# Performance work log

Measured on AMD Instinct MI355X. Metric: run time of the kernel, lower is better.

## Reference

```python
import jax, jax.numpy as jnp
import numpy as np
from jax import lax

# Faithful JAX translation of ConvAttention (enc=True, mask=False), the core
# kernel-headroom op of Conv_Transformer. Key observation: the per-(s,t)-pair
# conv2 over concat(Q[...,s], K[...,t]) is linear, so it decomposes exactly as
# conv(Q_s, W_q) + conv(K_t, W_k) + bias, where W_q/W_k are the first/second
# half of conv2's input channels. This reproduces the same math without
# materializing the [b, 2c, h, w, s, t] tensor or looping over time.

B, C, H, W, S = 4, 64, 64, 64, 20
K_SIZE = 3


def _conv_same(x, w):
    # x: [N, Cin, H, W], w: [Cout, Cin, kh, kw]
    return lax.conv_general_dilated(
        x, w, window_strides=(1, 1), padding='SAME',
        dimension_numbers=('NCHW', 'OIHW', 'NCHW'))


def setup_inputs() -> dict:
    key = jax.random.key(0)
    k1, k2, k3, k4, k5 = jax.random.split(key, 5)
    x = jax.random.normal(k1, (B, C, H, W, S), dtype=jnp.float32)
    w1 = jax.random.normal(k2, (3 * C, C, 1, 1), dtype=jnp.float32) * 0.05
    b1 = jax.random.normal(k3, (3 * C,), dtype=jnp.float32) * 0.05
    w2 = jax.random.normal(k4, (1, 2 * C, K_SIZE, K_SIZE), dtype=jnp.float32) * 0.05
    b2 = jax.random.normal(k5, (1,), dtype=jnp.float32) * 0.05
    return {'x': x, 'w1': w1, 'b1': b1, 'w2': w2, 'b2': b2}


def reference(x, w1, b1, w2, b2):
    b, c, h, w, s = x.shape
    # conv1 (1x1) per timestep -> QKV: [b, 3c, h, w, s]
    qkv = jnp.einsum('bchws,oc->bohws', x, w1[:, :, 0, 0]) \
        + b1[None, :, None, None, None]
    Q, K, V = jnp.split(qkv, 3, axis=1)  # each [b, c, h, w, s]

    # Decompose conv2 over concatenated channels.
    Wq, Wk = w2[:, :c], w2[:, c:]  # each [1, c, kh, kw]

    def per_time_conv(t5, wgt):
        # t5: [b, c, h, w, s] -> scores [b, h, w, s]
        flat = jnp.moveaxis(t5, -1, 1).reshape(b * s, c, h, w)
        out = _conv_same(flat, wgt)  # [b*s, 1, h, w]
        return out.reshape(b, s, h, w).transpose(0, 2, 3, 1)

    A = per_time_conv(Q, Wq)  # [b, h, w, s]  (query index)
    Bk = per_time_conv(K, Wk)  # [b, h, w, t]  (key index)

    # score[b,h,w,t,s] = conv2(concat(Q_s, K_t)) ; softmax over t (keys)
    scores = A[:, :, :, None, :] + Bk[:, :, :, :, None] + b2[0]
    attn = jax.nn.softmax(scores, axis=-2)  # [b, h, w, t, s]

    # V_out[b,c,h,w,s] = sum_t attn[...,t,s] * V[...,t]
    V_out = jnp.einsum('bhwts,bchwt->bchws', attn, V)
    return V_out
```

## Files before the change

kernel.cpp:

```cpp
#include <hip/hip_runtime.h>
#include <math.h>

#define Bb 4
#define Cc 64
#define Hh 64
#define Ww 64
#define Ss 20

constexpr int XC = Hh * Ww * Ss;
constexpr int XH = Ww * Ss;
constexpr int XW = Ss;
constexpr int XB = Cc * XC;
constexpr int NSITE = Bb * Hh * Ww;
constexpr int BKPLANE = NSITE * Ss;


__global__ void ct_fold_weights(const float* __restrict__ w1,
                                const float* __restrict__ b1,
                                const float* __restrict__ w2,
                                float* __restrict__ ws) {
    int tid = threadIdx.x;
    if (tid < 576) {
        int tap = tid >> 6, cp = tid & 63;
        float acc = 0.f;
        #pragma unroll 8
        for (int c = 0; c < 64; ++c)
            acc += w2[(64 + c) * 9 + tap] * w1[(64 + c) * 64 + cp];
        ws[tid] = acc;
    } else if (tid < 585) {
        int tap = tid - 576;
        float acc = 0.f;
        for (int c = 0; c < 64; ++c)
            acc += w2[(64 + c) * 9 + tap] * b1[64 + c];
        ws[576 + tap] = acc;
    }
}

template<int NPART>
__global__ __launch_bounds__(320) void ct_conv_bk(
        const float* __restrict__ x,
        const float* __restrict__ ws,
        float* __restrict__ bk) {
    __shared__ float weff[576];
    __shared__ float btap[9];
    int tid = threadIdx.x;
    for (int i = tid; i < 576; i += 320) weff[i] = ws[i];
    if (tid < 9) btap[tid] = ws[576 + tid];
    __syncthreads();

    constexpr int NCP = 64 / NPART;
    constexpr int CHUNK = 256 * NPART / 8;
    int g = (blockIdx.x & 7) * CHUNK + (blockIdx.x >> 3);
    int part = g >> 8;
    int nl = g & 255;
    int b = nl >> 6, h = nl & 63;
    int w = tid / 5, t4 = tid % 5;

    float vmask[9];
    int off[9];
    #pragma unroll
    for (int dh = 0; dh < 3; ++dh) {
        int hh = h + dh - 1;
        float hv = (hh >= 0 && hh < Hh) ? 1.f : 0.f;
        int hc = hh < 0 ? 0 : (hh > Hh - 1 ? Hh - 1 : hh);
        #pragma unroll
        for (int dw = 0; dw < 3; ++dw) {
            int wc = w + dw - 1;
            float wvd = (wc >= 0 && wc < Ww) ? 1.f : 0.f;
            int wcl = wc < 0 ? 0 : (wc > Ww - 1 ? Ww - 1 : wc);
            vmask[dh * 3 + dw] = hv * wvd;
            off[dh * 3 + dw] = hc * XH + wcl * XW;
        }
    }

    float bsum = 0.f;
    if (part == 0) {
        #pragma unroll
        for (int tap = 0; tap < 9; ++tap) bsum += btap[tap] * vmask[tap];
    }
    float4 acc = make_float4(bsum, bsum, bsum, bsum);

    const float* xb = x + b * XB + part * NCP * XC + t4 * 4;
    #pragma unroll 2
    for (int c = 0; c < NCP; ++c) {
        const float* xc = xb + c * XC;
        #pragma unroll
        for (int tap = 0; tap < 9; ++tap) {
            float wv = weff[tap * 64 + part * NCP + c] * vmask[tap];
            const float4 xv = *reinterpret_cast<const float4*>(xc + off[tap]);
            acc.x = fmaf(wv, xv.x, acc.x);
            acc.y = fmaf(wv, xv.y, acc.y);
            acc.z = fmaf(wv, xv.z, acc.z);
            acc.w = fmaf(wv, xv.w, acc.w);
        }
    }
    int site = nl * 64 + w;
    *reinterpret_cast<float4*>(bk + part * BKPLANE + site * 20 + t4 * 4) = acc;
}

template<int NPART>
__global__ __launch_bounds__(256) void ct_attn_out(
        const float* __restrict__ x,
        const float* __restrict__ w1,
        const float* __restrict__ b1,
        const float* __restrict__ bk,
        float* __restrict__ out) {
    __shared__ float w1t[64 * 65];
    __shared__ float psm[8][20];
    __shared__ float xsh[8][65];
    int tid = threadIdx.x;
    #pragma unroll
    for (int k = 0; k < 16; ++k) {
        int j = tid + k * 256;
        int r = j >> 6, q = j & 63;
        w1t[q * 65 + r] = w1[8192 + j];
    }

    int site0 = blockIdx.x * 8;

    if (tid < 160) {
        int si = tid / 20, i = tid % 20;
        float v = 0.f;
        #pragma unroll
        for (int pt = 0; pt < NPART; ++pt)
            v += bk[pt * BKPLANE + (site0 + si) * 20 + i];
        psm[si][i] = v;
    }
    __syncthreads();

    if (tid < 8) {
        float p[20];
        #pragma unroll
        for (int i = 0; i < 20; ++i) p[i] = psm[tid][i];
        float m = p[0];
        #pragma unroll
        for (int i = 1; i < 20; ++i) m = fmaxf(m, p[i]);
        float ssum = 0.f;
        #pragma unroll
        for (int i = 0; i < 20; ++i) { p[i] = __expf(p[i] - m); ssum += p[i]; }
        float inv = 1.f / ssum;
        #pragma unroll
        for (int i = 0; i < 20; ++i) psm[tid][i] = p[i] * inv;
    }
    __syncthreads();

    int si = tid & 7, cg = tid >> 3;
    int site = site0 + si;
    int b = site >> 12, hw = site & 4095;

    #pragma unroll
    for (int k = 0; k < 2; ++k) {
        int c = cg * 2 + k;
        const float* xp = x + (b * 64 + c) * XC + hw * 20;
        float xbv = 0.f;
        #pragma unroll
        for (int i = 0; i < 5; ++i) {
            float4 xv = reinterpret_cast<const float4*>(xp)[i];
            xbv = fmaf(psm[si][4 * i],     xv.x, xbv);
            xbv = fmaf(psm[si][4 * i + 1], xv.y, xbv);
            xbv = fmaf(psm[si][4 * i + 2], xv.z, xbv);
            xbv = fmaf(psm[si][4 * i + 3], xv.w, xbv);
        }
        xsh[si][c] = xbv;
    }
    __syncthreads();

    #pragma unroll
    for (int k = 0; k < 2; ++k) {
        int c = cg * 2 + k;
        float R = b1[128 + c];
        #pragma unroll 8
        for (int cp = 0; cp < 64; ++cp)
            R = fmaf(w1t[cp * 65 + c], xsh[si][cp], R);
        float* op = out + (b * 64 + c) * XC + hw * 20;
        float4 rv = make_float4(R, R, R, R);
        #pragma unroll
        for (int s4 = 0; s4 < 5; ++s4)
            reinterpret_cast<float4*>(op)[s4] = rv;
    }
}

extern "C" void kernel_launch(void* const* d_in, const int* in_sizes, int n_in,
                              void* d_out, int out_size, void* d_ws, size_t ws_size,
                              hipStream_t stream) {
    const float* x  = (const float*)d_in[0];
    const float* w1 = (const float*)d_in[1];
    const float* b1 = (const float*)d_in[2];
    const float* w2 = (const float*)d_in[3];
    float* ws    = (float*)d_ws;
    float* bkbuf = ws + 640;
    float* out   = (float*)d_out;

    ct_fold_weights<<<1, 640, 0, stream>>>(w1, b1, w2, ws);

    size_t need8 = (size_t)(640 + 8 * BKPLANE) * sizeof(float);
    size_t need4 = (size_t)(640 + 4 * BKPLANE) * sizeof(float);
    if (ws_size >= need8) {
        ct_conv_bk<8><<<2048, 320, 0, stream>>>(x, ws, bkbuf);
        ct_attn_out<8><<<2048, 256, 0, stream>>>(x, w1, b1, bkbuf, out);
    } else if (ws_size >= need4) {
        ct_conv_bk<4><<<1024, 320, 0, stream>>>(x, ws, bkbuf);
        ct_attn_out<4><<<2048, 256, 0, stream>>>(x, w1, b1, bkbuf, out);
    } else {
        ct_conv_bk<1><<<256, 320, 0, stream>>>(x, ws, bkbuf);
        ct_attn_out<1><<<2048, 256, 0, stream>>>(x, w1, b1, bkbuf, out);
    }
}
```

Before: 81.00 us.

## Replace 9-tap gather conv with row-streaming scatter conv over channel partitions

Adds a conv kernel that gives each block a 4-row strip of h. Every x row is loaded once and scattered into up to three output-row accumulators held in a register ring, instead of each output gathering nine taps with repeated loads. When the workspace is large enough it also splits channels into 16 partitions (4 channels each), so the partial sums are reduced in the attention kernel. This cuts redundant x loads in the conv but adds halo rows per strip and twice as many partial planes for the attention kernel to read.

New measurement: 73.81 us. 1.1x faster.

```diff
diff --git a/kernel.cpp b/kernel.cpp
--- a/kernel.cpp
+++ b/kernel.cpp
@@ -36,6 +36,106 @@
     }
 }
 
+template<int NCP>
+__global__ __launch_bounds__(320) void ct_conv_scatter(
+        const float* __restrict__ x,
+        const float* __restrict__ ws,
+        float* __restrict__ bk) {
+    constexpr int NPART = 64 / NCP;
+    constexpr int HT = 4;
+    constexpr int TOTAL = 4 * NPART * 16;
+    __shared__ float wsl[9 * NCP];
+    __shared__ float bt[9];
+    int tid = threadIdx.x;
+
+    int g = (blockIdx.x & 7) * (TOTAL / 8) + (blockIdx.x >> 3);
+    int hc = g & 15; g >>= 4;
+    int b = g & 3;
+    int part = g >> 2;
+
+    if (tid < 9 * NCP)
+        wsl[tid] = ws[(tid / NCP) * 64 + part * NCP + (tid % NCP)];
+    if (tid < 9) bt[tid] = ws[576 + tid];
+    __syncthreads();
+
+    int w = tid / 5, t4 = tid % 5;
+    int h0 = hc * HT;
+    float m0 = (w == 0)  ? 0.f : 1.f;
+    float m2 = (w == 63) ? 0.f : 1.f;
+    int wm1 = (w == 0) ? 0 : w - 1;
+    int wp1 = (w == 63) ? 63 : w + 1;
+    int cw0 = wm1 * XW, cw1 = w * XW, cw2 = wp1 * XW;
+
+    float bw0 = bt[0] * m0 + bt[1] + bt[2] * m2;
+    float bw1 = bt[3] * m0 + bt[4] + bt[5] * m2;
+    float bw2 = bt[6] * m0 + bt[7] + bt[8] * m2;
+    bool bias_on = (part == 0);
+
+    const float* xbase = x + b * XB + part * NCP * XC + t4 * 4;
+    float* bkp = bk + part * BKPLANE;
+
+    float4 ring[3];
+
+    #pragma unroll
+    for (int k = 0; k < HT + 2; ++k) {
+        if (k < HT) {
+            float bs = 0.f;
+            if (bias_on) {
+                int o = h0 + k;
+                bs = (o >= 1 ? bw0 : 0.f) + bw1 + (o + 1 < 64 ? bw2 : 0.f);
+            }
+            ring[k % 3] = make_float4(bs, bs, bs, bs);
+        }
+
+        int hr = h0 - 1 + k;
+        float4 xv[NCP][3];
+        if (hr >= 0 && hr < 64) {
+            #pragma unroll
+            for (int c = 0; c < NCP; ++c) {
+                const float* xr = xbase + c * XC + hr * XH;
+                xv[c][0] = *reinterpret_cast<const float4*>(xr + cw0);
+                xv[c][1] = *reinterpret_cast<const float4*>(xr + cw1);
+                xv[c][2] = *reinterpret_cast<const float4*>(xr + cw2);
+                xv[c][0].x *= m0; xv[c][0].y *= m0;
+                xv[c][0].z *= m0; xv[c][0].w *= m0;
+                xv[c][2].x *= m2; xv[c][2].y *= m2;
+                xv[c][2].z *= m2; xv[c][2].w *= m2;
+            }
+        } else {
+            #pragma unroll
+            for (int c = 0; c < NCP; ++c)
+                #pragma unroll
+                for (int dw = 0; dw < 3; ++dw)
+                    xv[c][dw] = make_float4(0.f, 0.f, 0.f, 0.f);
+        }
+
+        #pragma unroll
+        for (int dh = 0; dh < 3; ++dh) {
+            constexpr int dummy = 0; (void)dummy;
+            int off = k - dh;
+            if (off < 0 || off >= HT) continue;
+            int s = off % 3;
+            #pragma unroll
+            for (int c = 0; c < NCP; ++c) {
+                #pragma unroll
+                for (int dw = 0; dw < 3; ++dw) {
+                    float wv = wsl[(dh * 3 + dw) * NCP + c];
+                    ring[s].x = fmaf(wv, xv[c][dw].x, ring[s].x);
+                    ring[s].y = fmaf(wv, xv[c][dw].y, ring[s].y);
+                    ring[s].z = fmaf(wv, xv[c][dw].z, ring[s].z);
+                    ring[s].w = fmaf(wv, xv[c][dw].w, ring[s].w);
+                }
+            }
+        }
+
+        if (k >= 2) {
+            int o = h0 + k - 2;
+            int site = (b * 64 + o) * 64 + w;
+            *reinterpret_cast<float4*>(bkp + site * 20 + t4 * 4) = ring[(k - 2) % 3];
+        }
+    }
+}
+
 template<int NPART>
 __global__ __launch_bounds__(320) void ct_conv_bk(
         const float* __restrict__ x,
@@ -193,10 +293,14 @@
 
     ct_fold_weights<<<1, 640, 0, stream>>>(w1, b1, w2, ws);
 
-    size_t need8 = (size_t)(640 + 8 * BKPLANE) * sizeof(float);
-    size_t need4 = (size_t)(640 + 4 * BKPLANE) * sizeof(float);
-    if (ws_size >= need8) {
-        ct_conv_bk<8><<<2048, 320, 0, stream>>>(x, ws, bkbuf);
+    size_t need16 = (size_t)(640 + 16 * BKPLANE) * sizeof(float);
+    size_t need8  = (size_t)(640 + 8 * BKPLANE) * sizeof(float);
+    size_t need4  = (size_t)(640 + 4 * BKPLANE) * sizeof(float);
+    if (ws_size >= need16) {
+        ct_conv_scatter<4><<<1024, 320, 0, stream>>>(x, ws, bkbuf);
+        ct_attn_out<16><<<2048, 256, 0, stream>>>(x, w1, b1, bkbuf, out);
+    } else if (ws_size >= need8) {
+        ct_conv_scatter<8><<<512, 320, 0, stream>>>(x, ws, bkbuf);
         ct_attn_out<8><<<2048, 256, 0, stream>>>(x, w1, b1, bkbuf, out);
     } else if (ws_size >= need4) {
         ct_conv_bk<4><<<1024, 320, 0, stream>>>(x, ws, bkbuf);
```
